# Kernel tuning notes

Hardware: AMD Instinct MI355X
Metric: run time of the kernel (lower is better)

Reference implementation:

```python
import jax, jax.numpy as jnp
import numpy as np

N_NODES = 50000
N_EDGES = 800000
IN_CH = 128
OUT_CH = 64
HEADS = 4
NEG_SLOPE = 0.2


def setup_inputs() -> dict:
    key = jax.random.key(0)
    k1, k2, k3, k4, k5 = jax.random.split(key, 5)
    x = jax.random.normal(k1, (N_NODES, IN_CH), dtype=jnp.float32)
    edge_index = jax.random.randint(k2, (2, N_EDGES), 0, N_NODES, dtype=jnp.int64)
    # Glorot-ish scaled params
    W = jax.random.normal(k3, (IN_CH, HEADS * OUT_CH), dtype=jnp.float32) * (1.0 / np.sqrt(IN_CH))
    att_src = jax.random.normal(k4, (HEADS, OUT_CH), dtype=jnp.float32) * (1.0 / np.sqrt(OUT_CH))
    att_dst = jax.random.normal(k5, (HEADS, OUT_CH), dtype=jnp.float32) * (1.0 / np.sqrt(OUT_CH))
    bias = jnp.zeros((HEADS * OUT_CH,), dtype=jnp.float32)
    return {"x": x, "edge_index": edge_index, "W": W, "att_src": att_src, "att_dst": att_dst, "bias": bias}


def reference(x, edge_index, W, att_src, att_dst, bias):
    N = x.shape[0]
    H, C = att_src.shape
    # PyG GATConv default add_self_loops=True
    loops = jnp.arange(N, dtype=edge_index.dtype)
    src = jnp.concatenate([edge_index[0], loops])  # message source j
    dst = jnp.concatenate([edge_index[1], loops])  # message target i
    # Linear transform per head: [N, H, C]
    h = (x @ W).reshape(N, H, C)
    # Per-node attention logits: [N, H]
    a_src = jnp.sum(h * att_src[None], axis=-1)
    a_dst = jnp.sum(h * att_dst[None], axis=-1)
    # Per-edge raw score (alpha_src from source node, alpha_dst from target node)
    e = jax.nn.leaky_relu(a_src[src] + a_dst[dst], NEG_SLOPE)  # [E, H]
    # Segment-softmax over incoming edges of each target node
    m = jax.ops.segment_max(e, dst, num_segments=N)  # [N, H]
    m = jnp.where(jnp.isfinite(m), m, 0.0)  # nodes with no edges -> 0
    ex = jnp.exp(e - m[dst])
    denom = jax.ops.segment_sum(ex, dst, num_segments=N)  # [N, H]
    alpha = ex / (denom[dst] + 1e-16)  # [E, H]
    # Weighted aggregate of source features: [N, H, C]
    msg = h[src] * alpha[:, :, None]
    out = jax.ops.segment_sum(msg, dst, num_segments=N)
    # concat=True: flatten heads, add bias
    return out.reshape(N, H * C) + bias
```

## Files before the change

### kernel.cpp

```cpp
#include <hip/hip_runtime.h>

#define N_NODES 50000
#define N_EDGES 800000
#define IN_CH 128
#define OUT_CH 64
#define HEADS 4
#define HC 256
#define NEG_SLOPE 0.2f

#define HB_OFF       0UL
#define WSW_OFF      25600000UL
#define ASRC_OFF     25665536UL
#define ADST_OFF     26465536UL
#define COUNTS_OFF   27265536UL
#define OFFSETS_OFF  27465536UL
#define CURSOR_OFF   27665536UL
#define BSUMS_OFF    27865536UL
#define CSR_OFF      27866560UL

typedef __attribute__((ext_vector_type(8))) short short8;
typedef __attribute__((ext_vector_type(4))) float f32x4;

__device__ __forceinline__ unsigned short f2bf(float f) {
  unsigned int u = __float_as_uint(f);
  unsigned int r = (u + 0x7fffu + ((u >> 16) & 1u)) >> 16;
  return (unsigned short)r;
}
__device__ __forceinline__ float bf2f_lo(unsigned int u) {
  return __uint_as_float(u << 16);
}
__device__ __forceinline__ float bf2f_hi(unsigned int u) {
  return __uint_as_float(u & 0xffff0000u);
}

__global__ __launch_bounds__(256) void swizzle_W(const float* __restrict__ W,
                                                 unsigned short* __restrict__ Wsw) {
  int idx = blockIdx.x * 256 + threadIdx.x;
  if (idx >= 4096) return;
  int l = idx & 63;
  int kc = (idx >> 6) & 3;
  int t = idx >> 8;
  int kbase = kc * 32 + (l >> 4) * 8;
  int col = t * 16 + (l & 15);
  unsigned int p[4];
#pragma unroll
  for (int j = 0; j < 4; ++j) {
    unsigned int lo = f2bf(W[(size_t)(kbase + 2 * j) * HC + col]);
    unsigned int hi = f2bf(W[(size_t)(kbase + 2 * j + 1) * HC + col]);
    p[j] = lo | (hi << 16);
  }
  *(uint4*)(Wsw + (size_t)idx * 8) = make_uint4(p[0], p[1], p[2], p[3]);
}

__global__ __launch_bounds__(256) void gemm_mfma(const float* __restrict__ x,
                                                 const unsigned short* __restrict__ Wsw,
                                                 const float* __restrict__ att_s,
                                                 const float* __restrict__ att_d,
                                                 unsigned short* __restrict__ hb,
                                                 float* __restrict__ a_src,
                                                 float* __restrict__ a_dst) {
  __shared__ float Cs[4][16][256];
  const int wave = threadIdx.x >> 6;
  const int l = threadIdx.x & 63;
  const int q = l >> 4;
  const int m = l & 15;
  const int mrow = blockIdx.x * 64 + wave * 16 + m;
  const bool mvalid = mrow < N_NODES;
  const int rc = mvalid ? mrow : (N_NODES - 1);

  short8 a[4];
  const float* xr = x + (size_t)rc * IN_CH + q * 8;
#pragma unroll
  for (int kc = 0; kc < 4; ++kc) {
    float4 u = *(const float4*)(xr + kc * 32);
    float4 v = *(const float4*)(xr + kc * 32 + 4);
    short8 t;
    t[0] = (short)f2bf(u.x); t[1] = (short)f2bf(u.y);
    t[2] = (short)f2bf(u.z); t[3] = (short)f2bf(u.w);
    t[4] = (short)f2bf(v.x); t[5] = (short)f2bf(v.y);
    t[6] = (short)f2bf(v.z); t[7] = (short)f2bf(v.w);
    a[kc] = t;
  }

#pragma unroll
  for (int t = 0; t < 16; ++t) {
    f32x4 acc = {0.f, 0.f, 0.f, 0.f};
#pragma unroll
    for (int kc = 0; kc < 4; ++kc) {
      short8 b = *(const short8*)(Wsw + ((size_t)(t * 4 + kc) * 64 + l) * 8);
      acc = __builtin_amdgcn_mfma_f32_16x16x32_bf16(a[kc], b, acc, 0, 0, 0);
    }
#pragma unroll
    for (int r = 0; r < 4; ++r) {
      int row = q * 4 + r;
      Cs[wave][row][(t * 16 + m) ^ (row << 2)] = acc[r];
    }
  }
  __syncthreads();

  float as = 0.f, ad = 0.f;
  unsigned short* hrow = hb + (size_t)mrow * HC + q * 64;
  const int sw = m << 2;
#pragma unroll
  for (int i = 0; i < 8; ++i) {
    int col0 = q * 64 + i * 8;
    float4 c1 = *(const float4*)&Cs[wave][m][(col0) ^ sw];
    float4 c2 = *(const float4*)&Cs[wave][m][(col0 + 4) ^ sw];
    float4 s1 = *(const float4*)(att_s + col0);
    float4 s2 = *(const float4*)(att_s + col0 + 4);
    float4 d1 = *(const float4*)(att_d + col0);
    float4 d2 = *(const float4*)(att_d + col0 + 4);
    as += c1.x * s1.x + c1.y * s1.y + c1.z * s1.z + c1.w * s1.w;
    as += c2.x * s2.x + c2.y * s2.y + c2.z * s2.z + c2.w * s2.w;
    ad += c1.x * d1.x + c1.y * d1.y + c1.z * d1.z + c1.w * d1.w;
    ad += c2.x * d2.x + c2.y * d2.y + c2.z * d2.z + c2.w * d2.w;
    if (mvalid) {
      uint4 p;
      p.x = (unsigned int)f2bf(c1.x) | ((unsigned int)f2bf(c1.y) << 16);
      p.y = (unsigned int)f2bf(c1.z) | ((unsigned int)f2bf(c1.w) << 16);
      p.z = (unsigned int)f2bf(c2.x) | ((unsigned int)f2bf(c2.y) << 16);
      p.w = (unsigned int)f2bf(c2.z) | ((unsigned int)f2bf(c2.w) << 16);
      *(uint4*)(hrow + i * 8) = p;
    }
  }
  if (mvalid) {
    a_src[mrow * HEADS + q] = as;
    a_dst[mrow * HEADS + q] = ad;
  }
}

__global__ __launch_bounds__(256) void count_k(const int* __restrict__ dst,
                                               int* __restrict__ counts) {
  int e = blockIdx.x * 256 + threadIdx.x;
  if (e < N_EDGES) atomicAdd(&counts[dst[e]], 1);
}

__global__ __launch_bounds__(256) void scan1(const int* __restrict__ counts,
                                             int* __restrict__ offsets,
                                             int* __restrict__ bsums) {
  __shared__ int sd[256];
  const int base = blockIdx.x * 1024;
  const int t = threadIdx.x;
  int v[4];
  int tsum = 0;
#pragma unroll
  for (int k = 0; k < 4; ++k) {
    int i = base + t * 4 + k;
    v[k] = (i < N_NODES) ? counts[i] : 0;
    tsum += v[k];
  }
  sd[t] = tsum;
  __syncthreads();
  for (int off = 1; off < 256; off <<= 1) {
    int xval = (t >= off) ? sd[t - off] : 0;
    __syncthreads();
    sd[t] += xval;
    __syncthreads();
  }
  int excl = sd[t] - tsum;
  int run = excl;
#pragma unroll
  for (int k = 0; k < 4; ++k) {
    int i = base + t * 4 + k;
    if (i < N_NODES) offsets[i] = run;
    run += v[k];
  }
  if (t == 255) bsums[blockIdx.x] = sd[255];
}

__global__ void scan2(int* __restrict__ bsums, int nb) {
  if (threadIdx.x == 0 && blockIdx.x == 0) {
    int run = 0;
    for (int b = 0; b < nb; ++b) {
      int t = bsums[b];
      bsums[b] = run;
      run += t;
    }
  }
}

__global__ __launch_bounds__(256) void scan3(int* __restrict__ offsets,
                                             const int* __restrict__ bsums,
                                             int* __restrict__ cursor) {
  const int base = blockIdx.x * 1024;
  const int t = threadIdx.x;
  int add = bsums[blockIdx.x];
#pragma unroll
  for (int k = 0; k < 4; ++k) {
    int i = base + t * 4 + k;
    if (i < N_NODES) {
      int o = offsets[i] + add;
      offsets[i] = o;
      cursor[i] = o;
    }
  }
}

__global__ __launch_bounds__(256) void scatter_k(const int* __restrict__ src,
                                                 const int* __restrict__ dst,
                                                 int* __restrict__ cursor,
                                                 int* __restrict__ csr) {
  int e = blockIdx.x * 256 + threadIdx.x;
  if (e < N_EDGES) {
    int d = dst[e];
    int pos = atomicAdd(&cursor[d], 1);
    csr[pos] = src[e];
  }
}

__global__ __launch_bounds__(256) void aggregate(const unsigned short* __restrict__ hb,
                                                 const float* __restrict__ a_src,
                                                 const float* __restrict__ a_dst,
                                                 const int* __restrict__ counts,
                                                 const int* __restrict__ offsets,
                                                 const int* __restrict__ csr,
                                                 const float* __restrict__ bias,
                                                 float* __restrict__ out) {
  const int node = blockIdx.x * 4 + (threadIdx.x >> 6);
  const int l = threadIdx.x & 63;
  const int g = l >> 5;
  const int q = l & 31;
  const int hd = q >> 3;
  const int c0 = q * 8;
  const int deg = counts[node];
  const int start = offsets[node];
  const float adst = a_dst[node * HEADS + hd];

  float e_self = a_src[node * HEADS + hd] + adst;
  e_self = e_self > 0.f ? e_self : NEG_SLOPE * e_self;

  float mx = e_self;
  for (int j = g * 8 + (q & 7); j < deg; j += 16) {
    int s = csr[start + j];
    float e = a_src[s * HEADS + hd] + adst;
    e = e > 0.f ? e : NEG_SLOPE * e;
    mx = fmaxf(mx, e);
  }
  mx = fmaxf(mx, __shfl_xor(mx, 1));
  mx = fmaxf(mx, __shfl_xor(mx, 2));
  mx = fmaxf(mx, __shfl_xor(mx, 4));
  mx = fmaxf(mx, __shfl_xor(mx, 32));

  float denom = 0.f;
  float acc[8] = {0.f, 0.f, 0.f, 0.f, 0.f, 0.f, 0.f, 0.f};
#pragma unroll 2
  for (int j = 0; j + g < deg; j += 2) {
    int s = csr[start + j + g];
    float e = a_src[s * HEADS + hd] + adst;
    e = e > 0.f ? e : NEG_SLOPE * e;
    float ex = __expf(e - mx);
    denom += ex;
    uint4 hv = *(const uint4*)(hb + (size_t)s * HC + c0);
    acc[0] += bf2f_lo(hv.x) * ex;
    acc[1] += bf2f_hi(hv.x) * ex;
    acc[2] += bf2f_lo(hv.y) * ex;
    acc[3] += bf2f_hi(hv.y) * ex;
    acc[4] += bf2f_lo(hv.z) * ex;
    acc[5] += bf2f_hi(hv.z) * ex;
    acc[6] += bf2f_lo(hv.w) * ex;
    acc[7] += bf2f_hi(hv.w) * ex;
  }
  denom += __shfl_xor(denom, 32);
#pragma unroll
  for (int k = 0; k < 8; ++k) acc[k] += __shfl_xor(acc[k], 32);

  float ex_self = __expf(e_self - mx);
  denom += ex_self;
  uint4 hs = *(const uint4*)(hb + (size_t)node * HC + c0);
  acc[0] += bf2f_lo(hs.x) * ex_self;
  acc[1] += bf2f_hi(hs.x) * ex_self;
  acc[2] += bf2f_lo(hs.y) * ex_self;
  acc[3] += bf2f_hi(hs.y) * ex_self;
  acc[4] += bf2f_lo(hs.z) * ex_self;
  acc[5] += bf2f_hi(hs.z) * ex_self;
  acc[6] += bf2f_lo(hs.w) * ex_self;
  acc[7] += bf2f_hi(hs.w) * ex_self;

  if (g == 0) {
    float inv = 1.f / (denom + 1e-16f);
    float4 b1 = *(const float4*)(bias + c0);
    float4 b2 = *(const float4*)(bias + c0 + 4);
    float4 o1 = make_float4(acc[0] * inv + b1.x, acc[1] * inv + b1.y,
                            acc[2] * inv + b1.z, acc[3] * inv + b1.w);
    float4 o2 = make_float4(acc[4] * inv + b2.x, acc[5] * inv + b2.y,
                            acc[6] * inv + b2.z, acc[7] * inv + b2.w);
    *(float4*)(out + (size_t)node * HC + c0) = o1;
    *(float4*)(out + (size_t)node * HC + c0 + 4) = o2;
  }
}

extern "C" void kernel_launch(void* const* d_in, const int* in_sizes, int n_in,
                              void* d_out, int out_size, void* d_ws, size_t ws_size,
                              hipStream_t stream) {
  const float* x     = (const float*)d_in[0];
  const int*   ei    = (const int*)d_in[1];
  const float* W     = (const float*)d_in[2];
  const float* att_s = (const float*)d_in[3];
  const float* att_d = (const float*)d_in[4];
  const float* bias  = (const float*)d_in[5];
  float* out = (float*)d_out;

  char* ws = (char*)d_ws;
  unsigned short* hb  = (unsigned short*)(ws + HB_OFF);
  unsigned short* Wsw = (unsigned short*)(ws + WSW_OFF);
  float* a_src  = (float*)(ws + ASRC_OFF);
  float* a_dst  = (float*)(ws + ADST_OFF);
  int* counts   = (int*)(ws + COUNTS_OFF);
  int* offsets  = (int*)(ws + OFFSETS_OFF);
  int* cursor   = (int*)(ws + CURSOR_OFF);
  int* bsums    = (int*)(ws + BSUMS_OFF);
  int* csr      = (int*)(ws + CSR_OFF);

  const int* src = ei;
  const int* dst = ei + N_EDGES;

  hipMemsetAsync(counts, 0, N_NODES * sizeof(int), stream);

  swizzle_W<<<16, 256, 0, stream>>>(W, Wsw);
  gemm_mfma<<<782, 256, 0, stream>>>(x, Wsw, att_s, att_d, hb, a_src, a_dst);
  count_k<<<3125, 256, 0, stream>>>(dst, counts);
  scan1<<<49, 256, 0, stream>>>(counts, offsets, bsums);
  scan2<<<1, 64, 0, stream>>>(bsums, 49);
  scan3<<<49, 256, 0, stream>>>(offsets, bsums, cursor);
  scatter_k<<<3125, 256, 0, stream>>>(src, dst, cursor, csr);
  aggregate<<<12500, 256, 0, stream>>>(hb, a_src, a_dst, counts, offsets, csr, bias, out);
}
```

Baseline: 272.3 us.

## Fuse edge counting into GEMM launch and precompute edge exponentials in scatter

The degree-count kernel is merged into the GEMM launch as extra blocks, which removes one launch and lets the atomics overlap with GEMM work. The scatter pass now computes exp(leaky_relu(a_src+a_dst)) for each edge and stores it alongside the CSR entry. The aggregate kernel then reads these values directly, so the max-reduction pass and the per-edge exponential are gone. Dropping the max subtraction risks overflow in exp for large logits, and the extra edge-weight buffer adds memory traffic in both scatter and aggregate.

```diff
diff --git a/kernel.cpp b/kernel.cpp
--- a/kernel.cpp
+++ b/kernel.cpp
@@ -7,6 +7,8 @@
 #define HEADS 4
 #define HC 256
 #define NEG_SLOPE 0.2f
+#define GEMM_BLOCKS 782
+#define COUNT_BLOCKS 782
 
 #define HB_OFF       0UL
 #define WSW_OFF      25600000UL
@@ -17,6 +19,7 @@
 #define CURSOR_OFF   27665536UL
 #define BSUMS_OFF    27865536UL
 #define CSR_OFF      27866560UL
+#define EXV_OFF      31066560UL
 
 typedef __attribute__((ext_vector_type(8))) short short8;
 typedef __attribute__((ext_vector_type(4))) float f32x4;
@@ -31,6 +34,9 @@
 }
 __device__ __forceinline__ float bf2f_hi(unsigned int u) {
   return __uint_as_float(u & 0xffff0000u);
+}
+__device__ __forceinline__ float lrelu(float e) {
+  return e > 0.f ? e : NEG_SLOPE * e;
 }
 
 __global__ __launch_bounds__(256) void swizzle_W(const float* __restrict__ W,
@@ -52,14 +58,27 @@
   *(uint4*)(Wsw + (size_t)idx * 8) = make_uint4(p[0], p[1], p[2], p[3]);
 }
 
-__global__ __launch_bounds__(256) void gemm_mfma(const float* __restrict__ x,
-                                                 const unsigned short* __restrict__ Wsw,
-                                                 const float* __restrict__ att_s,
-                                                 const float* __restrict__ att_d,
-                                                 unsigned short* __restrict__ hb,
-                                                 float* __restrict__ a_src,
-                                                 float* __restrict__ a_dst) {
+__global__ __launch_bounds__(256) void gemm_count(const float* __restrict__ x,
+                                                  const unsigned short* __restrict__ Wsw,
+                                                  const float* __restrict__ att_s,
+                                                  const float* __restrict__ att_d,
+                                                  const int* __restrict__ dstv,
+                                                  unsigned short* __restrict__ hb,
+                                                  float* __restrict__ a_src,
+                                                  float* __restrict__ a_dst,
+                                                  int* __restrict__ counts) {
   __shared__ float Cs[4][16][256];
+
+  if (blockIdx.x >= GEMM_BLOCKS) {
+    int base = (blockIdx.x - GEMM_BLOCKS) * 1024 + threadIdx.x;
+#pragma unroll
+    for (int k = 0; k < 4; ++k) {
+      int e = base + k * 256;
+      if (e < N_EDGES) atomicAdd(&counts[dstv[e]], 1);
+    }
+    return;
+  }
+
   const int wave = threadIdx.x >> 6;
   const int l = threadIdx.x & 63;
   const int q = l >> 4;
@@ -129,12 +148,6 @@
   }
 }
 
-__global__ __launch_bounds__(256) void count_k(const int* __restrict__ dst,
-                                               int* __restrict__ counts) {
-  int e = blockIdx.x * 256 + threadIdx.x;
-  if (e < N_EDGES) atomicAdd(&counts[dst[e]], 1);
-}
-
 __global__ __launch_bounds__(256) void scan1(const int* __restrict__ counts,
                                              int* __restrict__ offsets,
                                              int* __restrict__ bsums) {
@@ -198,13 +211,25 @@
 
 __global__ __launch_bounds__(256) void scatter_k(const int* __restrict__ src,
                                                  const int* __restrict__ dst,
+                                                 const float* __restrict__ a_src,
+                                                 const float* __restrict__ a_dst,
                                                  int* __restrict__ cursor,
-                                                 int* __restrict__ csr) {
+                                                 int* __restrict__ csr,
+                                                 float* __restrict__ exv) {
   int e = blockIdx.x * 256 + threadIdx.x;
   if (e < N_EDGES) {
+    int s = src[e];
     int d = dst[e];
+    float4 as = *(const float4*)(a_src + s * 4);
+    float4 ad = *(const float4*)(a_dst + d * 4);
+    float4 ex;
+    ex.x = __expf(lrelu(as.x + ad.x));
+    ex.y = __expf(lrelu(as.y + ad.y));
+    ex.z = __expf(lrelu(as.z + ad.z));
+    ex.w = __expf(lrelu(as.w + ad.w));
     int pos = atomicAdd(&cursor[d], 1);
-    csr[pos] = src[e];
+    csr[pos] = s;
+    *(float4*)(exv + (size_t)pos * 4) = ex;
   }
 }
 
@@ -214,6 +239,7 @@
                                                  const int* __restrict__ counts,
                                                  const int* __restrict__ offsets,
                                                  const int* __restrict__ csr,
+                                                 const float* __restrict__ exv,
                                                  const float* __restrict__ bias,
                                                  float* __restrict__ out) {
   const int node = blockIdx.x * 4 + (threadIdx.x >> 6);
@@ -224,33 +250,16 @@
   const int c0 = q * 8;
   const int deg = counts[node];
   const int start = offsets[node];
-  const float adst = a_dst[node * HEADS + hd];
-
-  float e_self = a_src[node * HEADS + hd] + adst;
-  e_self = e_self > 0.f ? e_self : NEG_SLOPE * e_self;
-
-  float mx = e_self;
-  for (int j = g * 8 + (q & 7); j < deg; j += 16) {
-    int s = csr[start + j];
-    float e = a_src[s * HEADS + hd] + adst;
-    e = e > 0.f ? e : NEG_SLOPE * e;
-    mx = fmaxf(mx, e);
-  }
-  mx = fmaxf(mx, __shfl_xor(mx, 1));
-  mx = fmaxf(mx, __shfl_xor(mx, 2));
-  mx = fmaxf(mx, __shfl_xor(mx, 4));
-  mx = fmaxf(mx, __shfl_xor(mx, 32));
 
   float denom = 0.f;
   float acc[8] = {0.f, 0.f, 0.f, 0.f, 0.f, 0.f, 0.f, 0.f};
 #pragma unroll 2
   for (int j = 0; j + g < deg; j += 2) {
-    int s = csr[start + j + g];
-    float e = a_src[s * HEADS + hd] + adst;
-    e = e > 0.f ? e : NEG_SLOPE * e;
-    float ex = __expf(e - mx);
+    int idx = start + j + g;
+    int s = csr[idx];
+    float ex = exv[(size_t)idx * 4 + hd];
+    uint4 hv = *(const uint4*)(hb + (size_t)s * HC + c0);
     denom += ex;
-    uint4 hv = *(const uint4*)(hb + (size_t)s * HC + c0);
     acc[0] += bf2f_lo(hv.x) * ex;
     acc[1] += bf2f_hi(hv.x) * ex;
     acc[2] += bf2f_lo(hv.y) * ex;
@@ -264,7 +273,8 @@
 #pragma unroll
   for (int k = 0; k < 8; ++k) acc[k] += __shfl_xor(acc[k], 32);
 
-  float ex_self = __expf(e_self - mx);
+  float es = a_src[node * HEADS + hd] + a_dst[node * HEADS + hd];
+  float ex_self = __expf(lrelu(es));
   denom += ex_self;
   uint4 hs = *(const uint4*)(hb + (size_t)node * HC + c0);
   acc[0] += bf2f_lo(hs.x) * ex_self;
@@ -310,6 +320,7 @@
   int* cursor   = (int*)(ws + CURSOR_OFF);
   int* bsums    = (int*)(ws + BSUMS_OFF);
   int* csr      = (int*)(ws + CSR_OFF);
+  float* exv    = (float*)(ws + EXV_OFF);
 
   const int* src = ei;
   const int* dst = ei + N_EDGES;
@@ -317,11 +328,11 @@
   hipMemsetAsync(counts, 0, N_NODES * sizeof(int), stream);
 
   swizzle_W<<<16, 256, 0, stream>>>(W, Wsw);
-  gemm_mfma<<<782, 256, 0, stream>>>(x, Wsw, att_s, att_d, hb, a_src, a_dst);
-  count_k<<<3125, 256, 0, stream>>>(dst, counts);
+  gemm_count<<<GEMM_BLOCKS + COUNT_BLOCKS, 256, 0, stream>>>(
+      x, Wsw, att_s, att_d, dst, hb, a_src, a_dst, counts);
   scan1<<<49, 256, 0, stream>>>(counts, offsets, bsums);
   scan2<<<1, 64, 0, stream>>>(bsums, 49);
   scan3<<<49, 256, 0, stream>>>(offsets, bsums, cursor);
-  scatter_k<<<3125, 256, 0, stream>>>(src, dst, cursor, csr);
-  aggregate<<<12500, 256, 0, stream>>>(hb, a_src, a_dst, counts, offsets, csr, bias, out);
-}
+  scatter_k<<<3125, 256, 0, stream>>>(src, dst, a_src, a_dst, cursor, csr, exv);
+  aggregate<<<12500, 256, 0, stream>>>(hb, a_src, a_dst, counts, offsets, csr, exv, bias, out);
+}
```

New measurement: 263.6 us. -3.2%, faster.
